# Optimization experiments

Measured on AMD Instinct MI355X. Metric: run time of the kernel, lower is better.

The kernel has to match this reference:

```python
import jax, jax.numpy as jnp
import numpy as np
import math

N_ENTITIES = 200000
N_ITEMS = 100000
N_REL = 40
DIM = 64
N_HEADS = 2
DK = DIM // N_HEADS
N_EDGES = 1500000
K_EDGES = 256
K_ITEMS = 100


def setup_inputs() -> dict:
    key = jax.random.key(0)
    k1, k2, k3, k4, k5, k6 = jax.random.split(key, 6)
    entity_emb = jax.random.normal(k1, (N_ENTITIES, DIM), jnp.float32) * 0.1
    W_Q = jax.random.normal(k2, (DIM, DIM), jnp.float32) * (1.0 / math.sqrt(DIM))
    relation_emb = jax.random.normal(k3, (N_REL - 1, DIM), jnp.float32) * 0.1
    edge_index = jax.random.randint(k4, (2, N_EDGES), 0, N_ENTITIES, jnp.int32)
    # edge_type in [1, N_REL-1]: code indexes relation_emb[edge_type - 1]
    edge_type = jax.random.randint(k5, (N_EDGES,), 1, N_REL, jnp.int32)
    # uniform(0,1) driving the gumbel noise -log(-log(u)); clipped away from 0
    noise_u = jax.random.uniform(k6, (N_EDGES,), jnp.float32, 1e-9, 1.0)
    return {"entity_emb": entity_emb, "W_Q": W_Q, "relation_emb": relation_emb,
            "noise_u": noise_u, "edge_index": edge_index, "edge_type": edge_type}


def reference(entity_emb, W_Q, relation_emb, noise_u, edge_index, edge_type):
    head, tail = edge_index[0], edge_index[1]
    E = edge_index.shape[1]

    # --- norm_attn_computer (AttnHGCN): per-edge multi-head attention ---
    # project once on nodes, then gather (same math as (emb[head] @ W_Q))
    proj = entity_emb @ W_Q                               # [N, D]
    q = proj[head].reshape(E, N_HEADS, DK)                # [E, H, Dk]
    k = proj[tail].reshape(E, N_HEADS, DK)                # [E, H, Dk]
    rel = relation_emb[edge_type - 1].reshape(E, N_HEADS, DK)
    attn = jnp.sum(q * k * rel, axis=-1) / math.sqrt(DK)  # [E, H]
    edge_attn_logits = attn.mean(axis=-1)                 # [E]

    # scatter_softmax over head nodes, then multiply by head degree (norm)
    seg_max = jax.lax.stop_gradient(
        jax.ops.segment_max(edge_attn_logits, head, num_segments=N_ENTITIES))
    ex = jnp.exp(edge_attn_logits - seg_max[head])
    denom = jax.ops.segment_sum(ex, head, num_segments=N_ENTITIES)
    edge_attn_score = ex / denom[head]
    deg = jax.ops.segment_sum(jnp.ones_like(edge_attn_logits), head,
                              num_segments=N_ENTITIES)
    edge_attn_score = edge_attn_score * deg[head]         # [E]

    # --- attn logit sums per item (head + tail scatter_sum), topk 100 ---
    sum_by_node = (jax.ops.segment_sum(edge_attn_logits, head, num_segments=N_ENTITIES)
                   + jax.ops.segment_sum(edge_attn_logits, tail, num_segments=N_ENTITIES))
    top_items_v, top_attn_items = jax.lax.top_k(sum_by_node[:N_ITEMS], K_ITEMS)

    # --- gumbel-noise injection + edge topk 256 ---
    noisy_score = edge_attn_score + (-jnp.log(-jnp.log(noise_u)))
    topk_v, topk_attn_edge_id = jax.lax.top_k(noisy_score, K_EDGES)

    return (edge_attn_score, topk_v, topk_attn_edge_id, top_items_v, top_attn_items)
```

## Files before the change

### kernel.cpp

```cpp
#include <hip/hip_runtime.h>

#define N_ENTITIES 200000
#define N_ITEMS    100000
#define DIM        64
#define N_EDGES    1500000
#define K_EDGES    256
#define K_ITEMS    100
#define SCALE      0.08838834764831845f

#define CAND_CAP   4096
#define NSCANB     ((N_ENTITIES + 255) / 256)

typedef unsigned long long u64;


__device__ __forceinline__ unsigned fkey(float x) {
    unsigned u = __float_as_uint(x);
    return (u & 0x80000000u) ? ~u : (u | 0x80000000u);
}
__device__ __forceinline__ float funkey(unsigned k) {
    return (k & 0x80000000u) ? __uint_as_float(k & 0x7fffffffu)
                             : __uint_as_float(~k);
}

__device__ __forceinline__ void lds_hist_add(unsigned* h, unsigned bin, bool valid, int lane) {
    bool need = valid;
    for (;;) {
        unsigned long long mask = __ballot(need);
        if (mask == 0ull) break;
        int leader = __ffsll(mask) - 1;
        unsigned lbin = __shfl(bin, leader, 64);
        bool same = need && (bin == lbin);
        unsigned long long grp = __ballot(same);
        if (lane == leader) atomicAdd(&h[lbin], (unsigned)__popcll(grp));
        need = need && !same;
    }
}

__device__ __forceinline__ unsigned select_digit(const unsigned* __restrict__ hist,
                                                 unsigned Keff, unsigned* above) {
    unsigned cum = 0;
    int b = 255;
    for (; b > 0; --b) {
        unsigned hb = hist[b];
        if (cum + hb >= Keff) break;
        cum += hb;
    }
    *above = cum;
    return (unsigned)b;
}

__global__ __launch_bounds__(256) void proj_kernel(const float* __restrict__ emb,
                                                   const float* __restrict__ W,
                                                   float* __restrict__ proj,
                                                   const int* __restrict__ head,
                                                   unsigned* __restrict__ degi,
                                                   unsigned* __restrict__ rank) {
    int e = blockIdx.x * blockDim.x + threadIdx.x;
    unsigned rk = 0;
    bool haveEdge = (e < N_EDGES);
    if (haveEdge) rk = atomicAdd(&degi[head[e]], 1u);

    __shared__ float part[4][16][64];
    const int t = threadIdx.x;
    const int c = t & 63;
    const int q = __builtin_amdgcn_readfirstlane(t >> 6);

    float Wreg[16];
#pragma unroll
    for (int j = 0; j < 16; ++j) Wreg[j] = W[(q * 16 + j) * 64 + c];

    const int base = blockIdx.x * 16;
    const float* erow = emb + (size_t)base * 64 + q * 16;

    float acc[16];
#pragma unroll
    for (int r = 0; r < 16; ++r) acc[r] = 0.f;
#pragma unroll
    for (int r = 0; r < 16; ++r) {
#pragma unroll
        for (int j = 0; j < 16; ++j)
            acc[r] += erow[r * 64 + j] * Wreg[j];
    }
#pragma unroll
    for (int r = 0; r < 16; ++r) part[q][r][c] = acc[r];
    __syncthreads();
#pragma unroll
    for (int it = 0; it < 4; ++it) {
        int oi = t + it * 256;
        int r = oi >> 6, cc = oi & 63;
        float s = part[0][r][cc] + part[1][r][cc] + part[2][r][cc] + part[3][r][cc];
        proj[(size_t)(base + r) * 64 + cc] = s;
    }
    if (haveEdge) rank[e] = rk;
}

__global__ void scan1_kernel(const unsigned* __restrict__ degi, unsigned* __restrict__ start,
                             unsigned* __restrict__ bsum) {
    __shared__ unsigned s[256];
    int t = threadIdx.x, i = blockIdx.x * 256 + t;
    unsigned v = (i < N_ENTITIES) ? degi[i] : 0u;
    s[t] = v;
    __syncthreads();
    for (int off = 1; off < 256; off <<= 1) {
        unsigned x = s[t];
        unsigned y = (t >= off) ? s[t - off] : 0u;
        __syncthreads();
        s[t] = x + y;
        __syncthreads();
    }
    if (i < N_ENTITIES) start[i] = s[t] - v;
    if (t == 255) bsum[blockIdx.x] = s[t];
}

__global__ __launch_bounds__(256) void scan23_kernel(const unsigned* __restrict__ bsum,
                                                     unsigned* __restrict__ start) {
    __shared__ unsigned part[4];
    const int b = blockIdx.x;
    const int t = threadIdx.x;
    unsigned s = 0;
    for (int j = t; j < b; j += 256) s += bsum[j];
#pragma unroll
    for (int off = 1; off < 64; off <<= 1) s += __shfl_xor(s, off, 64);
    if ((t & 63) == 0) part[t >> 6] = s;
    __syncthreads();
    unsigned prefix = part[0] + part[1] + part[2] + part[3];
    int i = b * 256 + t;
    if (i < N_ENTITIES) start[i] += prefix;
}

__global__ void scatter_kernel(const int* __restrict__ head, const int* __restrict__ tail,
                               const int* __restrict__ etype,
                               unsigned* __restrict__ rank,
                               const unsigned* __restrict__ start,
                               u64* __restrict__ rec, int csrMode) {
    int i = blockIdx.x * blockDim.x + threadIdx.x;
    if (i >= N_EDGES) return;
    unsigned slot = start[head[i]] + rank[i];
    u64 R = ((u64)(unsigned)tail[i] << 27) | ((u64)(unsigned)(etype[i] - 1) << 21) | (u64)(unsigned)i;
    rec[slot] = R;
    if (csrMode) rank[i] = slot;
}

__global__ __launch_bounds__(256) void node_pass(const float4* __restrict__ proj4,
                                                 const float4* __restrict__ rel4,
                                                 const u64* __restrict__ rec,
                                                 const unsigned* __restrict__ start,
                                                 const unsigned* __restrict__ degi,
                                                 float* __restrict__ logitsOut,
                                                 int csrMode,
                                                 float2* __restrict__ nd,
                                                 float* __restrict__ sumhead,
                                                 float* __restrict__ sumtailR,
                                                 int repMask) {
    unsigned xcd;
    asm volatile("s_getreg_b32 %0, hwreg(HW_REG_XCC_ID)" : "=s"(xcd));
    float* st = sumtailR + (size_t)(xcd & (unsigned)repMask) * N_ITEMS;

    int wave = (blockIdx.x * blockDim.x + threadIdx.x) >> 6;
    int lane = threadIdx.x & 63;
    int slot = lane >> 4, sl = lane & 15;
    unsigned s = start[wave], len = degi[wave];
    float4 ph = proj4[(size_t)wave * 16 + sl];
    float dsum = 0.f, lsum = 0.f;
    for (unsigned k0 = 0; k0 < len; k0 += 16) {
        unsigned ka = k0 + slot, kb = ka + 4, kc = ka + 8, kd = ka + 12;
        bool va = (ka < len), vb = (kb < len), vc = (kc < len), vd = (kd < len);
        u64 Ra = rec[s + (va ? ka : 0u)];
        u64 Rb = rec[s + (vb ? kb : 0u)];
        u64 Rc = rec[s + (vc ? kc : 0u)];
        u64 Rd = rec[s + (vd ? kd : 0u)];
        unsigned ta = (unsigned)(Ra >> 27), ria = ((unsigned)(Ra >> 21)) & 63u;
        unsigned tb = (unsigned)(Rb >> 27), rib = ((unsigned)(Rb >> 21)) & 63u;
        unsigned tc = (unsigned)(Rc >> 27), ric = ((unsigned)(Rc >> 21)) & 63u;
        unsigned td = (unsigned)(Rd >> 27), rid = ((unsigned)(Rd >> 21)) & 63u;
        unsigned ea = (unsigned)Ra & 0x1FFFFFu, eb = (unsigned)Rb & 0x1FFFFFu;
        unsigned ec = (unsigned)Rc & 0x1FFFFFu, ed = (unsigned)Rd & 0x1FFFFFu;
        float4 pa = proj4[(size_t)ta * 16 + sl];
        float4 qa = rel4[(size_t)ria * 16 + sl];
        float4 pb = proj4[(size_t)tb * 16 + sl];
        float4 qb = rel4[(size_t)rib * 16 + sl];
        float4 pc = proj4[(size_t)tc * 16 + sl];
        float4 qc = rel4[(size_t)ric * 16 + sl];
        float4 pd = proj4[(size_t)td * 16 + sl];
        float4 qd = rel4[(size_t)rid * 16 + sl];
        float xa = ph.x * pa.x * qa.x + ph.y * pa.y * qa.y + ph.z * pa.z * qa.z + ph.w * pa.w * qa.w;
        float xb = ph.x * pb.x * qb.x + ph.y * pb.y * qb.y + ph.z * pb.z * qb.z + ph.w * pb.w * qb.w;
        float xc = ph.x * pc.x * qc.x + ph.y * pc.y * qc.y + ph.z * pc.z * qc.z + ph.w * pc.w * qc.w;
        float xd = ph.x * pd.x * qd.x + ph.y * pd.y * qd.y + ph.z * pd.z * qd.z + ph.w * pd.w * qd.w;
        xa += __shfl_xor(xa, 1, 64);  xb += __shfl_xor(xb, 1, 64);
        xc += __shfl_xor(xc, 1, 64);  xd += __shfl_xor(xd, 1, 64);
        xa += __shfl_xor(xa, 2, 64);  xb += __shfl_xor(xb, 2, 64);
        xc += __shfl_xor(xc, 2, 64);  xd += __shfl_xor(xd, 2, 64);
        xa += __shfl_xor(xa, 4, 64);  xb += __shfl_xor(xb, 4, 64);
        xc += __shfl_xor(xc, 4, 64);  xd += __shfl_xor(xd, 4, 64);
        xa += __shfl_xor(xa, 8, 64);  xb += __shfl_xor(xb, 8, 64);
        xc += __shfl_xor(xc, 8, 64);  xd += __shfl_xor(xd, 8, 64);
        if (sl == 0) {
            if (va) {
                float lg = xa * SCALE;
                logitsOut[csrMode ? (s + ka) : ea] = lg;
                dsum += __expf(lg);
                lsum += lg;
                if (ta < N_ITEMS) atomicAdd(&st[ta], lg);
            }
            if (vb) {
                float lg = xb * SCALE;
                logitsOut[csrMode ? (s + kb) : eb] = lg;
                dsum += __expf(lg);
                lsum += lg;
                if (tb < N_ITEMS) atomicAdd(&st[tb], lg);
            }
            if (vc) {
                float lg = xc * SCALE;
                logitsOut[csrMode ? (s + kc) : ec] = lg;
                dsum += __expf(lg);
                lsum += lg;
                if (tc < N_ITEMS) atomicAdd(&st[tc], lg);
            }
            if (vd) {
                float lg = xd * SCALE;
                logitsOut[csrMode ? (s + kd) : ed] = lg;
                dsum += __expf(lg);
                lsum += lg;
                if (td < N_ITEMS) atomicAdd(&st[td], lg);
            }
        }
    }
    dsum += __shfl_xor(dsum, 16, 64);
    dsum += __shfl_xor(dsum, 32, 64);
    lsum += __shfl_xor(lsum, 16, 64);
    lsum += __shfl_xor(lsum, 32, 64);
    if (lane == 0) {
        nd[wave] = make_float2(dsum, (float)len);
        sumhead[wave] = lsum;
    }
}

__global__ void edge_pass3(const float* __restrict__ logitsEdge,
                           const float* __restrict__ logitsCsr,
                           const unsigned* __restrict__ slotmap, int csrMode,
                           const int* __restrict__ head,
                           const float2* __restrict__ nd, const float* __restrict__ noise_u,
                           const float* __restrict__ sumhead, const float* __restrict__ sumtailR,
                           int R,
                           float* __restrict__ out_scores, unsigned* __restrict__ keysE,
                           unsigned* __restrict__ keysI, unsigned* __restrict__ hists) {
    __shared__ unsigned hE[256];
    __shared__ unsigned hI[256];
    for (int j = threadIdx.x; j < 256; j += blockDim.x) { hE[j] = 0; hI[j] = 0; }
    __syncthreads();
    int i = blockIdx.x * blockDim.x + threadIdx.x;
    int lane = threadIdx.x & 63;

    unsigned bin = 0;
    bool valid = (i < N_EDGES);
    if (valid) {
        float lg = csrMode ? logitsCsr[slotmap[i]] : logitsEdge[i];
        float2 dd = nd[head[i]];
        float score = __expf(lg) / dd.x * dd.y;
        out_scores[i] = score;
        float noise = -logf(-logf(noise_u[i]));
        unsigned k = fkey(score + noise);
        keysE[i] = k;
        bin = k >> 24;
    }
    lds_hist_add(hE, bin, valid, lane);

    bin = 0;
    valid = (i < N_ITEMS);
    if (valid) {
        float s = sumhead[i];
        for (int r = 0; r < R; ++r) s += sumtailR[(size_t)r * N_ITEMS + i];
        unsigned k = fkey(s);
        keysI[i] = k;
        bin = k >> 24;
    }
    lds_hist_add(hI, bin, valid, lane);

    __syncthreads();
    for (int j = threadIdx.x; j < 256; j += blockDim.x) {
        unsigned v = hE[j];
        if (v) atomicAdd(&hists[j], v);
        v = hI[j];
        if (v) atomicAdd(&hists[3 * 256 + j], v);
    }
}

__global__ void hist_stage_kernel(const unsigned* __restrict__ keysE,
                                  const unsigned* __restrict__ keysI,
                                  unsigned* __restrict__ hists, int stage) {
    __shared__ unsigned h[256];
    for (int j = threadIdx.x; j < 256; j += blockDim.x) h[j] = 0;
    __syncthreads();
    const int y = blockIdx.y;
    const unsigned* keys = y ? keysI : keysE;
    const int n = y ? N_ITEMS : N_EDGES;
    const unsigned K = y ? K_ITEMS : K_EDGES;
    unsigned* H = hists + (size_t)y * 3 * 256;

    unsigned aboveA, prefix;
    unsigned binA = select_digit(H, K, &aboveA);
    if (stage == 1) {
        prefix = binA;
    } else {
        unsigned aboveB;
        unsigned binB = select_digit(H + 256, K - aboveA, &aboveB);
        prefix = (binA << 8) | binB;
    }
    const int shift = 24 - 8 * stage;
    unsigned* out = H + stage * 256;

    const int lane = threadIdx.x & 63;
    const int stride = gridDim.x * blockDim.x;
    for (int idx = blockIdx.x * blockDim.x + threadIdx.x; idx - lane < n; idx += stride) {
        bool valid = (idx < n);
        unsigned bin = 0;
        if (valid) {
            unsigned k = keys[idx];
            if ((k >> (shift + 8)) != prefix) valid = false;
            bin = (k >> shift) & 0xFFu;
        }
        lds_hist_add(h, bin, valid, lane);
    }
    __syncthreads();
    for (int j = threadIdx.x; j < 256; j += blockDim.x) {
        unsigned v = h[j];
        if (v) atomicAdd(&out[j], v);
    }
}

__global__ void collect_kernel(const unsigned* __restrict__ keysE,
                               const unsigned* __restrict__ keysI,
                               const unsigned* __restrict__ hists,
                               unsigned* __restrict__ counters, unsigned* __restrict__ cand) {
    const int y = blockIdx.y;
    const unsigned* keys = y ? keysI : keysE;
    const int n = y ? N_ITEMS : N_EDGES;
    const unsigned K = y ? K_ITEMS : K_EDGES;
    const unsigned* H = hists + (size_t)y * 3 * 256;
    unsigned aboveA, aboveB, aboveC;
    unsigned binA = select_digit(H, K, &aboveA);
    unsigned binB = select_digit(H + 256, K - aboveA, &aboveB);
    unsigned binC = select_digit(H + 512, K - aboveA - aboveB, &aboveC);
    const unsigned T = ((binA << 16) | (binB << 8) | binC) << 8;
    unsigned* cd = cand + (size_t)y * 2 * CAND_CAP;

    int i = blockIdx.x * blockDim.x + threadIdx.x;
    int stride = gridDim.x * blockDim.x;
    for (; i < n; i += stride) {
        unsigned k = keys[i];
        if (k >= T) {
            unsigned p = atomicAdd(&counters[y], 1u);
            if (p < (unsigned)CAND_CAP) { cd[2 * p] = k; cd[2 * p + 1] = (unsigned)i; }
        }
    }
}

__global__ void final_topk_kernel(const unsigned* __restrict__ cand,
                                  const unsigned* __restrict__ counters,
                                  float* __restrict__ out_topkv, float* __restrict__ out_topki,
                                  float* __restrict__ out_itemv, float* __restrict__ out_itemi) {
    __shared__ unsigned sk[CAND_CAP];
    __shared__ unsigned si[CAND_CAP];
    const int y = blockIdx.x;
    const int K = y ? K_ITEMS : K_EDGES;
    float* outv = y ? out_itemv : out_topkv;
    float* outi = y ? out_itemi : out_topki;
    const unsigned* cd = cand + (size_t)y * 2 * CAND_CAP;
    unsigned m = counters[y];
    if (m > (unsigned)CAND_CAP) m = CAND_CAP;
    for (unsigned i = threadIdx.x; i < m; i += blockDim.x) {
        sk[i] = cd[2 * i];
        si[i] = cd[2 * i + 1];
    }
    __syncthreads();
    for (unsigned i = threadIdx.x; i < m; i += blockDim.x) {
        unsigned ki = sk[i], xi = si[i];
        int r = 0;
        for (unsigned j = 0; j < m; ++j) {
            unsigned kj = sk[j];
            if (kj > ki || (kj == ki && si[j] < xi)) r++;
        }
        if (r < K) {
            outv[r] = funkey(ki);
            outi[r] = (float)xi;
        }
    }
}

extern "C" void kernel_launch(void* const* d_in, const int* in_sizes, int n_in,
                              void* d_out, int out_size, void* d_ws, size_t ws_size,
                              hipStream_t stream) {
    (void)in_sizes; (void)n_in; (void)out_size;
    const float* emb    = (const float*)d_in[0];
    const float* W      = (const float*)d_in[1];
    const float* rel    = (const float*)d_in[2];
    const float* noise  = (const float*)d_in[3];
    const int*   eidx   = (const int*)d_in[4];
    const int*   etype  = (const int*)d_in[5];
    const int* head = eidx;
    const int* tail = eidx + N_EDGES;

    float* out        = (float*)d_out;
    float* out_scores = out;
    float* out_topkv  = out + N_EDGES;
    float* out_topki  = out + N_EDGES + K_EDGES;
    float* out_itemv  = out + N_EDGES + 2 * K_EDGES;
    float* out_itemi  = out + N_EDGES + 2 * K_EDGES + K_ITEMS;

    auto layout_floats = [](int R, int csr) -> size_t {
        return (size_t)N_ENTITIES * DIM + N_EDGES + 2 * (size_t)N_EDGES
             + N_ENTITIES + N_ENTITIES + (size_t)R * N_ITEMS
             + 2 * 3 * 256 + 2 + 2 * (size_t)N_ENTITIES + N_ENTITIES
             + 1024 + 2 * 2 * CAND_CAP + (csr ? (size_t)N_EDGES : 0);
    };
    int R = 8, csr = 1;
    while (R > 1 && ws_size < layout_floats(R, 1) * 4) R >>= 1;
    if (ws_size < layout_floats(1, 1) * 4) {
        csr = 0;
        R = 8;
        while (R > 1 && ws_size < layout_floats(R, 0) * 4) R >>= 1;
    }

    float* ws = (float*)d_ws;
    size_t o = 0;
    float*    proj    = ws + o;               o += (size_t)N_ENTITIES * DIM;
    unsigned* rank    = (unsigned*)(ws + o);
    float*    logits  = ws + o;               o += N_EDGES;
    u64*      rec     = (u64*)(ws + o);       o += 2 * (size_t)N_EDGES;
    unsigned* keysE   = (unsigned*)rec;
    unsigned* keysI   = keysE + N_EDGES;
    unsigned* start   = (unsigned*)(ws + o);  o += N_ENTITIES;
    unsigned* degi    = (unsigned*)(ws + o);  o += N_ENTITIES;
    float*    sumtailR= ws + o;               o += (size_t)R * N_ITEMS;
    unsigned* hists   = (unsigned*)(ws + o);  o += 2 * 3 * 256;
    unsigned* counters= (unsigned*)(ws + o);  o += 2;
    float2*   nd      = (float2*)(ws + o);    o += 2 * (size_t)N_ENTITIES;
    float*    sumhead = ws + o;               o += N_ENTITIES;
    unsigned* bsum    = (unsigned*)(ws + o);  o += 1024;
    unsigned* cand    = (unsigned*)(ws + o);  o += 2 * 2 * CAND_CAP;
    float*    logitsCsr = ws + o;             if (csr) o += N_EDGES;

    float*    nodePassLogits = csr ? logitsCsr : logits;

    hipMemsetAsync(degi, 0,
                   ((size_t)N_ENTITIES + (size_t)R * N_ITEMS + 2 * 3 * 256 + 2) * 4, stream);
    hipLaunchKernelGGL(proj_kernel, dim3(12500), dim3(256), 0, stream,
                       emb, W, proj, head, degi, rank);
    hipLaunchKernelGGL(scan1_kernel, dim3(NSCANB), dim3(256), 0, stream, degi, start, bsum);
    hipLaunchKernelGGL(scan23_kernel, dim3(NSCANB), dim3(256), 0, stream, bsum, start);
    hipLaunchKernelGGL(scatter_kernel, dim3((N_EDGES + 255) / 256), dim3(256), 0, stream,
                       head, tail, etype, rank, start, rec, csr);
    hipLaunchKernelGGL(node_pass, dim3(N_ENTITIES / 4), dim3(256), 0, stream,
                       (const float4*)proj, (const float4*)rel, rec, start, degi,
                       nodePassLogits, csr, nd, sumhead, sumtailR, R - 1);
    hipLaunchKernelGGL(edge_pass3, dim3((N_EDGES + 255) / 256), dim3(256), 0, stream,
                       logits, logitsCsr, rank, csr, head, (const float2*)nd, noise,
                       sumhead, sumtailR, R,
                       out_scores, keysE, keysI, hists);
    hipLaunchKernelGGL(hist_stage_kernel, dim3(512, 2), dim3(256), 0, stream,
                       keysE, keysI, hists, 1);
    hipLaunchKernelGGL(hist_stage_kernel, dim3(512, 2), dim3(256), 0, stream,
                       keysE, keysI, hists, 2);
    hipLaunchKernelGGL(collect_kernel, dim3(512, 2), dim3(256), 0, stream,
                       keysE, keysI, hists, counters, cand);
    hipLaunchKernelGGL(final_topk_kernel, dim3(2), dim3(1024), 0, stream,
                       cand, counters, out_topkv, out_topki, out_itemv, out_itemi);
}
```

Baseline: 512.9 us.

## Drop two radix histogram passes and halve node_pass edge unroll

The top-k selection now sets its candidate threshold from the first 8-bit digit histogram only. This removes the two extra hist_stage passes over the edge and item keys, and the candidate buffer is doubled to make room for the larger set. Separately, node_pass handles 2 edges per wave iteration instead of 4, which lowers register pressure but exposes less memory-level parallelism. The risk is that the top-byte bin holds more candidates than the cap, which would silently drop entries and give wrong top-k results, and final_topk has more candidates to sort.

```diff
diff --git a/kernel.cpp b/kernel.cpp
--- a/kernel.cpp
+++ b/kernel.cpp
@@ -8,7 +8,7 @@
 #define K_ITEMS    100
 #define SCALE      0.08838834764831845f
 
-#define CAND_CAP   4096
+#define CAND_CAP   8192
 #define NSCANB     ((N_ENTITIES + 255) / 256)
 
 typedef unsigned long long u64;
@@ -163,39 +163,24 @@
     unsigned s = start[wave], len = degi[wave];
     float4 ph = proj4[(size_t)wave * 16 + sl];
     float dsum = 0.f, lsum = 0.f;
-    for (unsigned k0 = 0; k0 < len; k0 += 16) {
-        unsigned ka = k0 + slot, kb = ka + 4, kc = ka + 8, kd = ka + 12;
-        bool va = (ka < len), vb = (kb < len), vc = (kc < len), vd = (kd < len);
+    for (unsigned k0 = 0; k0 < len; k0 += 8) {
+        unsigned ka = k0 + slot, kb = ka + 4;
+        bool va = (ka < len), vb = (kb < len);
         u64 Ra = rec[s + (va ? ka : 0u)];
         u64 Rb = rec[s + (vb ? kb : 0u)];
-        u64 Rc = rec[s + (vc ? kc : 0u)];
-        u64 Rd = rec[s + (vd ? kd : 0u)];
         unsigned ta = (unsigned)(Ra >> 27), ria = ((unsigned)(Ra >> 21)) & 63u;
         unsigned tb = (unsigned)(Rb >> 27), rib = ((unsigned)(Rb >> 21)) & 63u;
-        unsigned tc = (unsigned)(Rc >> 27), ric = ((unsigned)(Rc >> 21)) & 63u;
-        unsigned td = (unsigned)(Rd >> 27), rid = ((unsigned)(Rd >> 21)) & 63u;
         unsigned ea = (unsigned)Ra & 0x1FFFFFu, eb = (unsigned)Rb & 0x1FFFFFu;
-        unsigned ec = (unsigned)Rc & 0x1FFFFFu, ed = (unsigned)Rd & 0x1FFFFFu;
         float4 pa = proj4[(size_t)ta * 16 + sl];
         float4 qa = rel4[(size_t)ria * 16 + sl];
         float4 pb = proj4[(size_t)tb * 16 + sl];
         float4 qb = rel4[(size_t)rib * 16 + sl];
-        float4 pc = proj4[(size_t)tc * 16 + sl];
-        float4 qc = rel4[(size_t)ric * 16 + sl];
-        float4 pd = proj4[(size_t)td * 16 + sl];
-        float4 qd = rel4[(size_t)rid * 16 + sl];
         float xa = ph.x * pa.x * qa.x + ph.y * pa.y * qa.y + ph.z * pa.z * qa.z + ph.w * pa.w * qa.w;
         float xb = ph.x * pb.x * qb.x + ph.y * pb.y * qb.y + ph.z * pb.z * qb.z + ph.w * pb.w * qb.w;
-        float xc = ph.x * pc.x * qc.x + ph.y * pc.y * qc.y + ph.z * pc.z * qc.z + ph.w * pc.w * qc.w;
-        float xd = ph.x * pd.x * qd.x + ph.y * pd.y * qd.y + ph.z * pd.z * qd.z + ph.w * pd.w * qd.w;
         xa += __shfl_xor(xa, 1, 64);  xb += __shfl_xor(xb, 1, 64);
-        xc += __shfl_xor(xc, 1, 64);  xd += __shfl_xor(xd, 1, 64);
         xa += __shfl_xor(xa, 2, 64);  xb += __shfl_xor(xb, 2, 64);
-        xc += __shfl_xor(xc, 2, 64);  xd += __shfl_xor(xd, 2, 64);
         xa += __shfl_xor(xa, 4, 64);  xb += __shfl_xor(xb, 4, 64);
-        xc += __shfl_xor(xc, 4, 64);  xd += __shfl_xor(xd, 4, 64);
         xa += __shfl_xor(xa, 8, 64);  xb += __shfl_xor(xb, 8, 64);
-        xc += __shfl_xor(xc, 8, 64);  xd += __shfl_xor(xd, 8, 64);
         if (sl == 0) {
             if (va) {
                 float lg = xa * SCALE;
@@ -211,20 +196,6 @@
                 lsum += lg;
                 if (tb < N_ITEMS) atomicAdd(&st[tb], lg);
             }
-            if (vc) {
-                float lg = xc * SCALE;
-                logitsOut[csrMode ? (s + kc) : ec] = lg;
-                dsum += __expf(lg);
-                lsum += lg;
-                if (tc < N_ITEMS) atomicAdd(&st[tc], lg);
-            }
-            if (vd) {
-                float lg = xd * SCALE;
-                logitsOut[csrMode ? (s + kd) : ed] = lg;
-                dsum += __expf(lg);
-                lsum += lg;
-                if (td < N_ITEMS) atomicAdd(&st[td], lg);
-            }
         }
     }
     dsum += __shfl_xor(dsum, 16, 64);
@@ -287,49 +258,6 @@
     }
 }
 
-__global__ void hist_stage_kernel(const unsigned* __restrict__ keysE,
-                                  const unsigned* __restrict__ keysI,
-                                  unsigned* __restrict__ hists, int stage) {
-    __shared__ unsigned h[256];
-    for (int j = threadIdx.x; j < 256; j += blockDim.x) h[j] = 0;
-    __syncthreads();
-    const int y = blockIdx.y;
-    const unsigned* keys = y ? keysI : keysE;
-    const int n = y ? N_ITEMS : N_EDGES;
-    const unsigned K = y ? K_ITEMS : K_EDGES;
-    unsigned* H = hists + (size_t)y * 3 * 256;
-
-    unsigned aboveA, prefix;
-    unsigned binA = select_digit(H, K, &aboveA);
-    if (stage == 1) {
-        prefix = binA;
-    } else {
-        unsigned aboveB;
-        unsigned binB = select_digit(H + 256, K - aboveA, &aboveB);
-        prefix = (binA << 8) | binB;
-    }
-    const int shift = 24 - 8 * stage;
-    unsigned* out = H + stage * 256;
-
-    const int lane = threadIdx.x & 63;
-    const int stride = gridDim.x * blockDim.x;
-    for (int idx = blockIdx.x * blockDim.x + threadIdx.x; idx - lane < n; idx += stride) {
-        bool valid = (idx < n);
-        unsigned bin = 0;
-        if (valid) {
-            unsigned k = keys[idx];
-            if ((k >> (shift + 8)) != prefix) valid = false;
-            bin = (k >> shift) & 0xFFu;
-        }
-        lds_hist_add(h, bin, valid, lane);
-    }
-    __syncthreads();
-    for (int j = threadIdx.x; j < 256; j += blockDim.x) {
-        unsigned v = h[j];
-        if (v) atomicAdd(&out[j], v);
-    }
-}
-
 __global__ void collect_kernel(const unsigned* __restrict__ keysE,
                                const unsigned* __restrict__ keysI,
                                const unsigned* __restrict__ hists,
@@ -339,11 +267,9 @@
     const int n = y ? N_ITEMS : N_EDGES;
     const unsigned K = y ? K_ITEMS : K_EDGES;
     const unsigned* H = hists + (size_t)y * 3 * 256;
-    unsigned aboveA, aboveB, aboveC;
+    unsigned aboveA;
     unsigned binA = select_digit(H, K, &aboveA);
-    unsigned binB = select_digit(H + 256, K - aboveA, &aboveB);
-    unsigned binC = select_digit(H + 512, K - aboveA - aboveB, &aboveC);
-    const unsigned T = ((binA << 16) | (binB << 8) | binC) << 8;
+    const unsigned T = binA << 24;
     unsigned* cd = cand + (size_t)y * 2 * CAND_CAP;
 
     int i = blockIdx.x * blockDim.x + threadIdx.x;
@@ -459,10 +385,6 @@
                        logits, logitsCsr, rank, csr, head, (const float2*)nd, noise,
                        sumhead, sumtailR, R,
                        out_scores, keysE, keysI, hists);
-    hipLaunchKernelGGL(hist_stage_kernel, dim3(512, 2), dim3(256), 0, stream,
-                       keysE, keysI, hists, 1);
-    hipLaunchKernelGGL(hist_stage_kernel, dim3(512, 2), dim3(256), 0, stream,
-                       keysE, keysI, hists, 2);
     hipLaunchKernelGGL(collect_kernel, dim3(512, 2), dim3(256), 0, stream,
                        keysE, keysI, hists, counters, cand);
     hipLaunchKernelGGL(final_topk_kernel, dim3(2), dim3(1024), 0, stream,
```

Measured after the change: 504.7 us. Within noise of the previous version (-1.6%).
